# Performance work log

Hardware: AMD Instinct MI355X
Metric: run time of the kernel (lower is better)

Reference implementation:

```python
import jax, jax.numpy as jnp
import numpy as np

V = 50257   # vocab size
E = 256     # embedding_dimension
D = 8       # key_query_reduced_dimensionality
H = 8       # no_of_attention_heads
L = 16      # no_of_blocks
B = 8       # batch
T = 512     # seq len == context_size
FF = 4 * E  # MLP hidden


def setup_inputs() -> dict:
    key = jax.random.key(0)
    ks = jax.random.split(key, 12)
    rn = lambda k, s: jax.random.normal(k, s, jnp.float32) * 0.02
    return {
        'tokens': jax.random.randint(ks[0], (B, T), 0, V),
        'ideal_value': jax.random.randint(ks[1], (B, T), 0, V),
        'tok_emb': rn(ks[2], (V, E)),
        'pos_emb': rn(ks[3], (T, E)),
        'Wq': rn(ks[4], (L, H, E, D)),
        'Wk': rn(ks[5], (L, H, E, D)),
        'Wv': rn(ks[6], (L, H, E, D)),
        'Wo': rn(ks[7], (L, H * D, E)),
        'bo': jnp.zeros((L, E), jnp.float32),
        'ln1_s': jnp.ones((L, E), jnp.float32),
        'ln1_b': jnp.zeros((L, E), jnp.float32),
        'W1': rn(ks[8], (L, E, FF)),
        'b1': jnp.zeros((L, FF), jnp.float32),
        'W2': rn(ks[9], (L, FF, E)),
        'b2': jnp.zeros((L, E), jnp.float32),
        'ln2_s': jnp.ones((L, E), jnp.float32),
        'ln2_b': jnp.zeros((L, E), jnp.float32),
        'lnf_s': jnp.ones((E,), jnp.float32),
        'lnf_b': jnp.zeros((E,), jnp.float32),
        'Wf': rn(ks[10], (E, V)),
        'bf': jnp.zeros((V,), jnp.float32),
    }


def _ln(x, s, b):
    m = x.mean(-1, keepdims=True)
    v = ((x - m) ** 2).mean(-1, keepdims=True)
    return (x - m) * jax.lax.rsqrt(v + 1e-5) * s + b


def reference(tokens, ideal_value, tok_emb, pos_emb, Wq, Wk, Wv, Wo, bo,
              ln1_s, ln1_b, W1, b1, W2, b2, ln2_s, ln2_b, lnf_s, lnf_b, Wf, bf):
    Bn, Tn = tokens.shape
    x = tok_emb[tokens] + pos_emb[:Tn]                      # [B,T,E]
    # faithful mask: masked_fill where transpose(tril(R))==0 -> keep upper triangle
    keep = jnp.triu(jnp.ones((D, D), bool))
    scale = jnp.float32(E) ** 0.5

    def block(x, p):
        wq, wk, wv, wo, bo_, s1, bb1, w1, bm1, w2, bm2, s2, bb2 = p
        h = _ln(x, s1, bb1)
        Q = jnp.einsum('bte,hed->bhtd', h, wq)              # [B,H,T,D]
        K = jnp.einsum('bte,hed->bhtd', h, wk)
        Vv = jnp.einsum('bte,hed->bhtd', h, wv)
        # R = K^T @ Q : feature-by-feature [B,H,D,D] (this repo's quirky attention)
        R = jnp.einsum('bhti,bhtj->bhij', K, Q) / scale
        R = jax.nn.softmax(jnp.where(keep, R, -jnp.inf), axis=-1)
        a = jnp.einsum('bhti,bhij->bhtj', Vv, R)            # V @ R, [B,H,T,D]
        a = a.transpose(0, 2, 1, 3).reshape(x.shape[0], x.shape[1], H * D)
        x = x + a @ wo + bo_                                # dropout is identity (eval)
        h2 = _ln(x, s2, bb2)
        x = x + jax.nn.relu(h2 @ w1 + bm1) @ w2 + bm2
        return x, None

    x, _ = jax.lax.scan(block, x, (Wq, Wk, Wv, Wo, bo, ln1_s, ln1_b,
                                   W1, b1, W2, b2, ln2_s, ln2_b))
    logits = (_ln(x, lnf_s, lnf_b) @ Wf + bf).reshape(-1, V)  # [B*T, V]
    tgt = ideal_value.reshape(-1)
    logp = jax.nn.log_softmax(logits, axis=-1)
    loss = -jnp.take_along_axis(logp, tgt[:, None], axis=1).mean()
    return logits, loss
```

## Files before the change

kernel.cpp:

```cpp
#include <hip/hip_runtime.h>
#include <math.h>

#define V_SZ 50257
#define NPAD 50432
#define NCB 197

typedef short s16x8 __attribute__((ext_vector_type(8)));
typedef ushort u16x4 __attribute__((ext_vector_type(4)));
typedef float f32x4 __attribute__((ext_vector_type(4)));

__device__ __forceinline__ ushort f2bf(float x) {
    union { float f; unsigned u; } v; v.f = x;
    unsigned r = v.u + 0x7FFF + ((v.u >> 16) & 1);
    return (ushort)(r >> 16);
}
__device__ __forceinline__ float bf2f(ushort u) {
    union { unsigned u; float f; } v; v.u = ((unsigned)u) << 16; return v.f;
}

__global__ __launch_bounds__(256) void gpt_embed_ln(const int* __restrict__ tokens,
                                                    const float* __restrict__ tok_emb,
                                                    const float* __restrict__ pos_emb,
                                                    const float* __restrict__ s, const float* __restrict__ b,
                                                    float* __restrict__ x, ushort* __restrict__ hb) {
    int wave = threadIdx.x >> 6, lane = threadIdx.x & 63;
    int row = blockIdx.x * 4 + wave;
    int t = row & 511;
    int tok = tokens[row];
    float4 te = ((const float4*)(tok_emb + tok * 256))[lane];
    float4 pe = ((const float4*)(pos_emb + t * 256))[lane];
    float4 v = make_float4(te.x + pe.x, te.y + pe.y, te.z + pe.z, te.w + pe.w);
    ((float4*)(x + row * 256))[lane] = v;
    float sum = v.x + v.y + v.z + v.w;
    #pragma unroll
    for (int off = 1; off < 64; off <<= 1) sum += __shfl_xor(sum, off);
    float mean = sum * (1.0f / 256.0f);
    float dx = v.x - mean, dy = v.y - mean, dz = v.z - mean, dw = v.w - mean;
    float vs = dx * dx + dy * dy + dz * dz + dw * dw;
    #pragma unroll
    for (int off = 1; off < 64; off <<= 1) vs += __shfl_xor(vs, off);
    float rstd = rsqrtf(vs * (1.0f / 256.0f) + 1e-5f);
    float4 sv = ((const float4*)s)[lane];
    float4 bv = ((const float4*)b)[lane];
    u16x4 o;
    o[0] = f2bf(dx * rstd * sv.x + bv.x);
    o[1] = f2bf(dy * rstd * sv.y + bv.y);
    o[2] = f2bf(dz * rstd * sv.z + bv.z);
    o[3] = f2bf(dw * rstd * sv.w + bv.w);
    *(u16x4*)&hb[row * 256 + lane * 4] = o;
}

__global__ __launch_bounds__(256) void cvt_transpose(const float* __restrict__ in, ushort* __restrict__ out,
                                                     int Kd, int Nd, int n_real,
                                                     int in_stride, int out_stride) {
    __shared__ __align__(16) ushort t[64][80];
    const float* inp = in + (size_t)blockIdx.z * in_stride;
    ushort* outp = out + (size_t)blockIdx.z * out_stride;
    int n0 = blockIdx.x * 64, k0 = blockIdx.y * 64;
    int tid = threadIdx.x;
    #pragma unroll
    for (int p = 0; p < 4; p++) {
        int lk = p * 16 + (tid >> 4);
        int ln = (tid & 15) * 4;
        int k = k0 + lk, n = n0 + ln;
        const float* rowp = inp + (size_t)k * Nd;
        float v0 = 0.f, v1 = 0.f, v2 = 0.f, v3 = 0.f;
        if (n + 0 < n_real) v0 = rowp[n + 0];
        if (n + 1 < n_real) v1 = rowp[n + 1];
        if (n + 2 < n_real) v2 = rowp[n + 2];
        if (n + 3 < n_real) v3 = rowp[n + 3];
        t[ln + 0][lk] = f2bf(v0);
        t[ln + 1][lk] = f2bf(v1);
        t[ln + 2][lk] = f2bf(v2);
        t[ln + 3][lk] = f2bf(v3);
    }
    __syncthreads();
    int ln = tid >> 2, kq = (tid & 3) * 16;
    ushort* op = outp + (size_t)(n0 + ln) * Kd + k0 + kq;
    *(s16x8*)&op[0] = *(const s16x8*)&t[ln][kq];
    *(s16x8*)&op[8] = *(const s16x8*)&t[ln][kq + 8];
}

__global__ __launch_bounds__(256) void cvt_qkv(const float* __restrict__ Wq, const float* __restrict__ Wk,
                                               const float* __restrict__ Wv, ushort* __restrict__ WqkvT) {
    int l = blockIdx.x, kind = blockIdx.y;
    const float* W = (kind == 0 ? Wq : (kind == 1 ? Wk : Wv)) + l * 16384;
    ushort* out = WqkvT + (size_t)l * 65536 + kind * 64 * 256;
    int tid = threadIdx.x;
    #pragma unroll 4
    for (int it = 0; it < 64; it++) {
        int idx = it * 256 + tid;
        int row = idx >> 8, e = idx & 255;
        int h = row >> 3, d = row & 7;
        out[row * 256 + e] = f2bf(W[h * 2048 + e * 8 + d]);
    }
    if (kind == 0) {
        ushort* zp = WqkvT + (size_t)l * 65536 + 192 * 256;
        #pragma unroll 4
        for (int it = 0; it < 64; it++) zp[it * 256 + tid] = 0;
    }
}

__global__ __launch_bounds__(512, 4) void gpt_pre(const ushort* __restrict__ hb,
                                                  const ushort* __restrict__ WqkvT,
                                                  ushort* __restrict__ Vb,
                                                  float* __restrict__ Rpart) {
    __shared__ __align__(16) ushort As[16 * 64];
    __shared__ __align__(16) ushort Bs[256 * 64];
    __shared__ float kqv[16][193];
    const int tid = threadIdx.x, lane = tid & 63, wn = tid >> 6;
    const int rows0 = blockIdx.x * 16;
    const int fr = lane & 15, fkb = (lane >> 4) * 16;
    const int arow = tid >> 3, ach = tid & 7;

    f32x4 acc[2];
    acc[0] = (f32x4)0.0f; acc[1] = (f32x4)0.0f;

    s16x8 ra, rb[4];
    if (tid < 128) ra = *(const s16x8*)&hb[(size_t)(rows0 + arow) * 256 + ach * 8];
    #pragma unroll
    for (int i = 0; i < 4; i++) {
        int u = tid + i * 512, r = u >> 3, ch = u & 7;
        rb[i] = *(const s16x8*)&WqkvT[(size_t)r * 256 + ch * 8];
    }
    #pragma unroll 1
    for (int kt = 0; kt < 4; kt++) {
        if (kt) __syncthreads();
        if (tid < 128)
            *(s16x8*)&As[arow * 64 + (((ach * 16) ^ ((arow & 7) << 4)) >> 1)] = ra;
        #pragma unroll
        for (int i = 0; i < 4; i++) {
            int u = tid + i * 512, r = u >> 3, ch = u & 7;
            *(s16x8*)&Bs[r * 64 + (((ch * 16) ^ ((r & 7) << 4)) >> 1)] = rb[i];
        }
        __syncthreads();
        if (kt < 3) {
            int k0 = (kt + 1) * 64;
            if (tid < 128) ra = *(const s16x8*)&hb[(size_t)(rows0 + arow) * 256 + k0 + ach * 8];
            #pragma unroll
            for (int i = 0; i < 4; i++) {
                int u = tid + i * 512, r = u >> 3, ch = u & 7;
                rb[i] = *(const s16x8*)&WqkvT[(size_t)r * 256 + k0 + ch * 8];
            }
        }
        #pragma unroll
        for (int kk = 0; kk < 2; kk++) {
            int kbyte = kk * 64 + fkb;
            s16x8 af = *(const s16x8*)&As[fr * 64 + ((kbyte ^ ((fr & 7) << 4)) >> 1)];
            #pragma unroll
            for (int n = 0; n < 2; n++) {
                int brow = wn * 32 + n * 16 + fr;
                s16x8 bfv = *(const s16x8*)&Bs[brow * 64 + ((kbyte ^ ((brow & 7) << 4)) >> 1)];
                acc[n] = __builtin_amdgcn_mfma_f32_16x16x32_bf16(af, bfv, acc[n], 0, 0, 0);
            }
        }
    }
    #pragma unroll
    for (int n = 0; n < 2; n++) {
        int col = wn * 32 + n * 16 + fr;
        if (col < 192) {
            #pragma unroll
            for (int r = 0; r < 4; r++)
                kqv[(lane >> 4) * 4 + r][col] = acc[n][r];
        }
    }
    __syncthreads();
    #pragma unroll
    for (int i = 0; i < 2; i++) {
        int u = tid + i * 512, t = u >> 6, hd = u & 63;
        Vb[(size_t)(rows0 + t) * 64 + hd] = f2bf(kqv[t][128 + hd]);
    }
    {
        int h = tid >> 6, i2 = (tid >> 3) & 7, j = tid & 7;
        float s = 0.0f;
        #pragma unroll
        for (int t = 0; t < 16; t++)
            s += kqv[t][64 + h * 8 + i2] * kqv[t][h * 8 + j];
        int bb = rows0 >> 9, part = (rows0 >> 4) & 31;
        Rpart[(size_t)(bb * 32 + part) * 512 + tid] = s;
    }
}

__global__ __launch_bounds__(512, 4) void gpt_layer(
        const float* __restrict__ Rpart_in, const ushort* __restrict__ Vb_in,
        const ushort* __restrict__ WoT, const float* __restrict__ bo,
        const ushort* __restrict__ W1T, const float* __restrict__ b1,
        const ushort* __restrict__ W2T, const float* __restrict__ b2,
        const float* __restrict__ ls2, const float* __restrict__ lb2,
        const float* __restrict__ nls, const float* __restrict__ nlb,
        float* __restrict__ x,
        const ushort* __restrict__ WqkvT_next,
        ushort* __restrict__ Vb_out, float* __restrict__ Rpart_out,
        ushort* __restrict__ hbout, int mode) {
    __shared__ __align__(16) ushort Bs[256 * 64];
    __shared__ __align__(16) ushort ffs[16 * 1024];
    __shared__ __align__(16) ushort h2s[16 * 256];
    __shared__ __align__(16) ushort abl[16 * 64];
    __shared__ __align__(16) ushort Vl[16 * 64];
    __shared__ float Rs[512];
    __shared__ float red1[16][8], red2[16][8], mrow[16], rrow[16];

    const int tid = threadIdx.x, lane = tid & 63, wn = tid >> 6;
    const int rows0 = blockIdx.x * 16, b = rows0 >> 9;
    const int fr = lane & 15, fkb = (lane >> 4) * 16, rbase = (lane >> 4) * 4;
    int colv[2]; colv[0] = wn * 32 + fr; colv[1] = wn * 32 + 16 + fr;

    {
        const float* rp = Rpart_in + (size_t)b * 32 * 512 + tid;
        float s = 0.0f;
        #pragma unroll
        for (int p = 0; p < 32; p++) s += rp[p * 512];
        s *= (1.0f / 16.0f);
        int ii = (tid >> 3) & 7, j = tid & 7;
        float val = (j >= ii) ? s : -INFINITY;
        float m = val;
        #pragma unroll
        for (int off = 1; off < 8; off <<= 1) m = fmaxf(m, __shfl_xor(m, off, 8));
        float ex = __expf(val - m);
        float su = ex;
        #pragma unroll
        for (int off = 1; off < 8; off <<= 1) su += __shfl_xor(su, off, 8);
        Rs[tid] = ex / su;
    }
    #pragma unroll
    for (int i = 0; i < 2; i++) {
        int u = tid + i * 512, t = u >> 6, hd = u & 63;
        Vl[t * 64 + hd] = Vb_in[(size_t)(rows0 + t) * 64 + hd];
    }
    __syncthreads();
    #pragma unroll
    for (int i = 0; i < 2; i++) {
        int u = tid + i * 512, t = u >> 6, hd = u & 63, h = hd >> 3, j = hd & 7;
        float a = 0.0f;
        #pragma unroll
        for (int q = 0; q < 8; q++)
            a += bf2f(Vl[t * 64 + h * 8 + q]) * Rs[h * 64 + q * 8 + j];
        abl[t * 64 + (((hd * 2) ^ ((t & 7) << 4)) >> 1)] = f2bf(a);
    }
    s16x8 rbv[4];
    #pragma unroll
    for (int i = 0; i < 4; i++) {
        int u = tid + i * 512, r = u >> 3, ch = u & 7;
        rbv[i] = *(const s16x8*)&WoT[(size_t)r * 64 + ch * 8];
    }
    __syncthreads();
    #pragma unroll
    for (int i = 0; i < 4; i++) {
        int u = tid + i * 512, r = u >> 3, ch = u & 7;
        *(s16x8*)&Bs[r * 64 + (((ch * 16) ^ ((r & 7) << 4)) >> 1)] = rbv[i];
    }
    __syncthreads();
    f32x4 acc[2];
    acc[0] = (f32x4)0.0f; acc[1] = (f32x4)0.0f;
    #pragma unroll
    for (int kk = 0; kk < 2; kk++) {
        int kbyte = kk * 64 + fkb;
        s16x8 af = *(const s16x8*)&abl[fr * 64 + ((kbyte ^ ((fr & 7) << 4)) >> 1)];
        #pragma unroll
        for (int n = 0; n < 2; n++) {
            int brow = wn * 32 + n * 16 + fr;
            s16x8 bfv = *(const s16x8*)&Bs[brow * 64 + ((kbyte ^ ((brow & 7) << 4)) >> 1)];
            acc[n] = __builtin_amdgcn_mfma_f32_16x16x32_bf16(af, bfv, acc[n], 0, 0, 0);
        }
    }
    float xn[2][4];
    #pragma unroll
    for (int n = 0; n < 2; n++) {
        int col = colv[n];
        float bbv = bo[col];
        #pragma unroll
        for (int r = 0; r < 4; r++)
            xn[n][r] = acc[n][r] + bbv + x[(size_t)(rows0 + rbase + r) * 256 + col];
    }
    #pragma unroll
    for (int r = 0; r < 4; r++) {
        float s1 = xn[0][r] + xn[1][r];
        float s2 = xn[0][r] * xn[0][r] + xn[1][r] * xn[1][r];
        #pragma unroll
        for (int off = 1; off < 16; off <<= 1) {
            s1 += __shfl_xor(s1, off);
            s2 += __shfl_xor(s2, off);
        }
        if (fr == 0) { red1[rbase + r][wn] = s1; red2[rbase + r][wn] = s2; }
    }
    __syncthreads();
    if (tid < 16) {
        float s1 = 0.f, s2 = 0.f;
        #pragma unroll
        for (int w = 0; w < 8; w++) { s1 += red1[tid][w]; s2 += red2[tid][w]; }
        float mean = s1 * (1.0f / 256.0f);
        float var = s2 * (1.0f / 256.0f) - mean * mean;
        mrow[tid] = mean;
        rrow[tid] = rsqrtf(var + 1e-5f);
    }
    __syncthreads();
    #pragma unroll
    for (int n = 0; n < 2; n++) {
        int col = colv[n];
        float lsv = ls2[col], lbv = lb2[col];
        #pragma unroll
        for (int r = 0; r < 4; r++) {
            int rl = rbase + r;
            float hv = (xn[n][r] - mrow[rl]) * rrow[rl] * lsv + lbv;
            h2s[rl * 256 + (((col * 2) ^ ((rl & 7) << 4)) >> 1)] = f2bf(hv);
        }
    }
    #pragma unroll 1
    for (int c = 0; c < 4; c++) {
        const ushort* Bg = W1T + (size_t)c * 256 * 256;
        acc[0] = (f32x4)0.0f; acc[1] = (f32x4)0.0f;
        #pragma unroll
        for (int i = 0; i < 4; i++) {
            int u = tid + i * 512, r = u >> 3, ch = u & 7;
            rbv[i] = *(const s16x8*)&Bg[(size_t)r * 256 + ch * 8];
        }
        #pragma unroll 1
        for (int kt = 0; kt < 4; kt++) {
            __syncthreads();
            #pragma unroll
            for (int i = 0; i < 4; i++) {
                int u = tid + i * 512, r = u >> 3, ch = u & 7;
                *(s16x8*)&Bs[r * 64 + (((ch * 16) ^ ((r & 7) << 4)) >> 1)] = rbv[i];
            }
            __syncthreads();
            if (kt < 3) {
                int k0 = (kt + 1) * 64;
                #pragma unroll
                for (int i = 0; i < 4; i++) {
                    int u = tid + i * 512, r = u >> 3, ch = u & 7;
                    rbv[i] = *(const s16x8*)&Bg[(size_t)r * 256 + k0 + ch * 8];
                }
            }
            #pragma unroll
            for (int kk = 0; kk < 2; kk++) {
                int kbyte = kt * 128 + kk * 64 + fkb;
                s16x8 af = *(const s16x8*)&h2s[fr * 256 + ((kbyte ^ ((fr & 7) << 4)) >> 1)];
                int kb2 = kk * 64 + fkb;
                #pragma unroll
                for (int n = 0; n < 2; n++) {
                    int brow = wn * 32 + n * 16 + fr;
                    s16x8 bfv = *(const s16x8*)&Bs[brow * 64 + ((kb2 ^ ((brow & 7) << 4)) >> 1)];
                    acc[n] = __builtin_amdgcn_mfma_f32_16x16x32_bf16(af, bfv, acc[n], 0, 0, 0);
                }
            }
        }
        #pragma unroll
        for (int n = 0; n < 2; n++) {
            int col = c * 256 + colv[n];
            float bb1 = b1[col];
            #pragma unroll
            for (int r = 0; r < 4; r++) {
                int rl = rbase + r;
                ffs[rl * 1024 + (((col * 2) ^ ((rl & 7) << 4)) >> 1)] =
                    f2bf(fmaxf(acc[n][r] + bb1, 0.0f));
            }
        }
    }
    f32x4 a2[2];
    a2[0] = (f32x4)0.0f; a2[1] = (f32x4)0.0f;
    #pragma unroll
    for (int i = 0; i < 4; i++) {
        int u = tid + i * 512, r = u >> 3, ch = u & 7;
        rbv[i] = *(const s16x8*)&W2T[(size_t)r * 1024 + ch * 8];
    }
    #pragma unroll 1
    for (int kt = 0; kt < 16; kt++) {
        __syncthreads();
        #pragma unroll
        for (int i = 0; i < 4; i++) {
            int u = tid + i * 512, r = u >> 3, ch = u & 7;
            *(s16x8*)&Bs[r * 64 + (((ch * 16) ^ ((r & 7) << 4)) >> 1)] = rbv[i];
        }
        __syncthreads();
        if (kt < 15) {
            int k0 = (kt + 1) * 64;
            #pragma unroll
            for (int i = 0; i < 4; i++) {
                int u = tid + i * 512, r = u >> 3, ch = u & 7;
                rbv[i] = *(const s16x8*)&W2T[(size_t)r * 1024 + k0 + ch * 8];
            }
        }
        #pragma unroll
        for (int kk = 0; kk < 2; kk++) {
            int kbyte = kt * 128 + kk * 64 + fkb;
            s16x8 af = *(const s16x8*)&ffs[fr * 1024 + ((kbyte ^ ((fr & 7) << 4)) >> 1)];
            int kb2 = kk * 64 + fkb;
            #pragma unroll
            for (int n = 0; n < 2; n++) {
                int brow = wn * 32 + n * 16 + fr;
                s16x8 bfv = *(const s16x8*)&Bs[brow * 64 + ((kb2 ^ ((brow & 7) << 4)) >> 1)];
                a2[n] = __builtin_amdgcn_mfma_f32_16x16x32_bf16(af, bfv, a2[n], 0, 0, 0);
            }
        }
    }
    #pragma unroll
    for (int n = 0; n < 2; n++) {
        int col = colv[n];
        float bb2 = b2[col];
        #pragma unroll
        for (int r = 0; r < 4; r++) {
            float v = xn[n][r] + a2[n][r] + bb2;
            xn[n][r] = v;
            x[(size_t)(rows0 + rbase + r) * 256 + col] = v;
        }
    }
    __syncthreads();
    #pragma unroll
    for (int r = 0; r < 4; r++) {
        float s1 = xn[0][r] + xn[1][r];
        float s2 = xn[0][r] * xn[0][r] + xn[1][r] * xn[1][r];
        #pragma unroll
        for (int off = 1; off < 16; off <<= 1) {
            s1 += __shfl_xor(s1, off);
            s2 += __shfl_xor(s2, off);
        }
        if (fr == 0) { red1[rbase + r][wn] = s1; red2[rbase + r][wn] = s2; }
    }
    __syncthreads();
    if (tid < 16) {
        float s1 = 0.f, s2 = 0.f;
        #pragma unroll
        for (int w = 0; w < 8; w++) { s1 += red1[tid][w]; s2 += red2[tid][w]; }
        float mean = s1 * (1.0f / 256.0f);
        float var = s2 * (1.0f / 256.0f) - mean * mean;
        mrow[tid] = mean;
        rrow[tid] = rsqrtf(var + 1e-5f);
    }
    __syncthreads();
    #pragma unroll
    for (int n = 0; n < 2; n++) {
        int col = colv[n];
        float lsv = nls[col], lbv = nlb[col];
        #pragma unroll
        for (int r = 0; r < 4; r++) {
            int rl = rbase + r;
            float hv = (xn[n][r] - mrow[rl]) * rrow[rl] * lsv + lbv;
            ushort hu = f2bf(hv);
            h2s[rl * 256 + (((col * 2) ^ ((rl & 7) << 4)) >> 1)] = hu;
            if (mode == 0)
                hbout[(size_t)(rows0 + rl) * 256 + col] = hu;
        }
    }
    if (mode == 0) return;

    float* kqv = (float*)ffs;
    acc[0] = (f32x4)0.0f; acc[1] = (f32x4)0.0f;
    #pragma unroll
    for (int i = 0; i < 4; i++) {
        int u = tid + i * 512, r = u >> 3, ch = u & 7;
        rbv[i] = *(const s16x8*)&WqkvT_next[(size_t)r * 256 + ch * 8];
    }
    #pragma unroll 1
    for (int kt = 0; kt < 4; kt++) {
        __syncthreads();
        #pragma unroll
        for (int i = 0; i < 4; i++) {
            int u = tid + i * 512, r = u >> 3, ch = u & 7;
            *(s16x8*)&Bs[r * 64 + (((ch * 16) ^ ((r & 7) << 4)) >> 1)] = rbv[i];
        }
        __syncthreads();
        if (kt < 3) {
            int k0 = (kt + 1) * 64;
            #pragma unroll
            for (int i = 0; i < 4; i++) {
                int u = tid + i * 512, r = u >> 3, ch = u & 7;
                rbv[i] = *(const s16x8*)&WqkvT_next[(size_t)r * 256 + k0 + ch * 8];
            }
        }
        #pragma unroll
        for (int kk = 0; kk < 2; kk++) {
            int kbyte = kt * 128 + kk * 64 + fkb;
            s16x8 af = *(const s16x8*)&h2s[fr * 256 + ((kbyte ^ ((fr & 7) << 4)) >> 1)];
            int kb2 = kk * 64 + fkb;
            #pragma unroll
            for (int n = 0; n < 2; n++) {
                int brow = wn * 32 + n * 16 + fr;
                s16x8 bfv = *(const s16x8*)&Bs[brow * 64 + ((kb2 ^ ((brow & 7) << 4)) >> 1)];
                acc[n] = __builtin_amdgcn_mfma_f32_16x16x32_bf16(af, bfv, acc[n], 0, 0, 0);
            }
        }
    }
    __syncthreads();
    #pragma unroll
    for (int n = 0; n < 2; n++) {
        int col = wn * 32 + n * 16 + fr;
        if (col < 192) {
            #pragma unroll
            for (int r = 0; r < 4; r++)
                kqv[(rbase + r) * 193 + col] = acc[n][r];
        }
    }
    __syncthreads();
    #pragma unroll
    for (int i = 0; i < 2; i++) {
        int u = tid + i * 512, t = u >> 6, hd = u & 63;
        Vb_out[(size_t)(rows0 + t) * 64 + hd] = f2bf(kqv[t * 193 + 128 + hd]);
    }
    {
        int h = tid >> 6, i2 = (tid >> 3) & 7, j = tid & 7;
        float s = 0.0f;
        #pragma unroll
        for (int t = 0; t < 16; t++)
            s += kqv[t * 193 + 64 + h * 8 + i2] * kqv[t * 193 + h * 8 + j];
        int part = (rows0 >> 4) & 31;
        Rpart_out[(size_t)(b * 32 + part) * 512 + tid] = s;
    }
}

__global__ __launch_bounds__(512, 4) void gpt_logits_mfma(const ushort* __restrict__ hb, const ushort* __restrict__ WfT,
                                                          const float* __restrict__ bfb, float* __restrict__ out,
                                                          float2* __restrict__ lsebuf) {
    __shared__ __align__(16) ushort As[128 * 64];
    __shared__ __align__(16) ushort Bs[256 * 64];
    f32x4 acc[4][4];
    int flat = blockIdx.y * 32 + blockIdx.x;
    int nf = (flat & 7) * 788 + (flat >> 3);
    int rb = nf & 31, cb = nf >> 5;
    int row0 = rb * 128, c0 = cb * 256;
    const int tid = threadIdx.x, lane = tid & 63, wid = tid >> 6;
    const int wm = wid >> 2, wn = wid & 3;
    const int fr = lane & 15, fkb = (lane >> 4) * 16;

    #pragma unroll
    for (int m = 0; m < 4; m++)
        #pragma unroll
        for (int n = 0; n < 4; n++) acc[m][n] = (f32x4)0.0f;

    s16x8 ra[2], rbv[4];
    #pragma unroll
    for (int i = 0; i < 2; i++) {
        int u = tid + i * 512, r = u >> 3, ch = u & 7;
        ra[i] = *(const s16x8*)&hb[(size_t)(row0 + r) * 256 + ch * 8];
    }
    #pragma unroll
    for (int i = 0; i < 4; i++) {
        int u = tid + i * 512, r = u >> 3, ch = u & 7;
        rbv[i] = *(const s16x8*)&WfT[(size_t)(c0 + r) * 256 + ch * 8];
    }
    #pragma unroll 1
    for (int kt = 0; kt < 4; kt++) {
        if (kt) __syncthreads();
        #pragma unroll
        for (int i = 0; i < 2; i++) {
            int u = tid + i * 512, r = u >> 3, ch = u & 7;
            *(s16x8*)&As[r * 64 + (((ch * 16) ^ ((r & 7) << 4)) >> 1)] = ra[i];
        }
        #pragma unroll
        for (int i = 0; i < 4; i++) {
            int u = tid + i * 512, r = u >> 3, ch = u & 7;
            *(s16x8*)&Bs[r * 64 + (((ch * 16) ^ ((r & 7) << 4)) >> 1)] = rbv[i];
        }
        __syncthreads();
        if (kt < 3) {
            int k0 = (kt + 1) * 64;
            #pragma unroll
            for (int i = 0; i < 2; i++) {
                int u = tid + i * 512, r = u >> 3, ch = u & 7;
                ra[i] = *(const s16x8*)&hb[(size_t)(row0 + r) * 256 + k0 + ch * 8];
            }
            #pragma unroll
            for (int i = 0; i < 4; i++) {
                int u = tid + i * 512, r = u >> 3, ch = u & 7;
                rbv[i] = *(const s16x8*)&WfT[(size_t)(c0 + r) * 256 + k0 + ch * 8];
            }
        }
        #pragma unroll
        for (int kk = 0; kk < 2; kk++) {
            int kbyte = kk * 64 + fkb;
            s16x8 af[4], bfr[4];
            #pragma unroll
            for (int m = 0; m < 4; m++) {
                int arow = wm * 64 + m * 16 + fr;
                af[m] = *(const s16x8*)&As[arow * 64 + ((kbyte ^ ((arow & 7) << 4)) >> 1)];
            }
            #pragma unroll
            for (int n = 0; n < 4; n++) {
                int brow = wn * 64 + n * 16 + fr;
                bfr[n] = *(const s16x8*)&Bs[brow * 64 + ((kbyte ^ ((brow & 7) << 4)) >> 1)];
            }
            #pragma unroll
            for (int m = 0; m < 4; m++)
                #pragma unroll
                for (int n = 0; n < 4; n++)
                    acc[m][n] = __builtin_amdgcn_mfma_f32_16x16x32_bf16(af[m], bfr[n], acc[m][n], 0, 0, 0);
        }
    }
    float bb[4]; int gcv[4];
    #pragma unroll
    for (int n = 0; n < 4; n++) {
        int gc = c0 + wn * 64 + n * 16 + fr;
        gcv[n] = gc;
        bb[n] = (gc < V_SZ) ? bfb[gc] : 0.0f;
    }
    __syncthreads();
    float2 (*red)[4] = (float2(*)[4])As;
    #pragma unroll
    for (int m = 0; m < 4; m++) {
        int rloc = wm * 64 + m * 16 + (lane >> 4) * 4;
        int gr = row0 + rloc;
        #pragma unroll
        for (int r = 0; r < 4; r++) {
            float v[4];
            float vmax = -1e30f;
            #pragma unroll
            for (int n = 0; n < 4; n++) {
                v[n] = (gcv[n] < V_SZ) ? acc[m][n][r] + bb[n] : -1e30f;
                vmax = fmaxf(vmax, v[n]);
            }
            #pragma unroll
            for (int n = 0; n < 4; n++)
                if (gcv[n] < V_SZ)
                    out[(size_t)(gr + r) * V_SZ + gcv[n]] = v[n];
            #pragma unroll
            for (int off = 1; off < 16; off <<= 1)
                vmax = fmaxf(vmax, __shfl_xor(vmax, off));
            float vsum = __expf(v[0] - vmax) + __expf(v[1] - vmax)
                       + __expf(v[2] - vmax) + __expf(v[3] - vmax);
            #pragma unroll
            for (int off = 1; off < 16; off <<= 1)
                vsum += __shfl_xor(vsum, off);
            if ((lane & 15) == 0)
                red[rloc + r][wn] = make_float2(vmax, vsum);
        }
    }
    __syncthreads();
    if (tid < 128) {
        float M = -1e30f, S = 0.0f;
        #pragma unroll
        for (int w = 0; w < 4; w++) {
            float2 p = red[tid][w];
            float M2 = fmaxf(M, p.x);
            S = S * __expf(M - M2) + p.y * __expf(p.x - M2);
            M = M2;
        }
        lsebuf[(size_t)(row0 + tid) * NCB + cb] = make_float2(M, S);
    }
}

__global__ __launch_bounds__(256) void gpt_lse(const float2* __restrict__ lsebuf, const float* __restrict__ out,
                                               const int* __restrict__ tgt, float* __restrict__ partial) {
    int wave = threadIdx.x >> 6, lane = threadIdx.x & 63;
    int row = blockIdx.x * 4 + wave;
    float m = -INFINITY, s = 0.0f;
    for (int i = lane; i < NCB; i += 64) {
        float2 p = lsebuf[(size_t)row * NCB + i];
        float M = fmaxf(m, p.x);
        s = s * __expf(m - M) + p.y * __expf(p.x - M);
        m = M;
    }
    #pragma unroll
    for (int off = 1; off < 64; off <<= 1) {
        float m2 = __shfl_xor(m, off);
        float s2 = __shfl_xor(s, off);
        float M = fmaxf(m, m2);
        s = s * __expf(m - M) + s2 * __expf(m2 - M);
        m = M;
    }
    if (lane == 0)
        partial[row] = m + logf(s) - out[(size_t)row * V_SZ + tgt[row]];
}

__global__ void gpt_loss_reduce(const float* __restrict__ partial, float* __restrict__ out) {
    __shared__ float red[256];
    int tid = threadIdx.x;
    float s = 0.0f;
    for (int i = tid; i < 4096; i += 256) s += partial[i];
    red[tid] = s;
    __syncthreads();
    for (int off = 128; off > 0; off >>= 1) {
        if (tid < off) red[tid] += red[tid + off];
        __syncthreads();
    }
    if (tid == 0) out[0] = red[0] * (1.0f / 4096.0f);
}

__global__ void gpt_embed(const int* __restrict__ tokens, const float* __restrict__ tok_emb,
                          const float* __restrict__ pos_emb, float* __restrict__ x) {
    int idx = blockIdx.x * 256 + threadIdx.x;
    int bt = idx >> 8, e = idx & 255;
    int t = bt & 511;
    int tok = tokens[bt];
    x[idx] = tok_emb[tok * 256 + e] + pos_emb[t * 256 + e];
}

__global__ void gpt_ln(const float* __restrict__ x, const float* __restrict__ s,
                       const float* __restrict__ b, float* __restrict__ h) {
    __shared__ float red[256];
    int row = blockIdx.x, e = threadIdx.x;
    float v = x[row * 256 + e];
    red[e] = v;
    __syncthreads();
    for (int off = 128; off > 0; off >>= 1) {
        if (e < off) red[e] += red[e + off];
        __syncthreads();
    }
    float mean = red[0] * (1.0f / 256.0f);
    __syncthreads();
    float d = v - mean;
    red[e] = d * d;
    __syncthreads();
    for (int off = 128; off > 0; off >>= 1) {
        if (e < off) red[e] += red[e + off];
        __syncthreads();
    }
    float rstd = rsqrtf(red[0] * (1.0f / 256.0f) + 1e-5f);
    h[row * 256 + e] = d * rstd * s[e] + b[e];
}

__global__ void gpt_qkv(const float* __restrict__ h, const float* __restrict__ Wq,
                        const float* __restrict__ Wk, const float* __restrict__ Wv,
                        float* __restrict__ Q, float* __restrict__ K, float* __restrict__ Vv) {
    __shared__ float hs[8][256];
    int tid = threadIdx.x;
    int row0 = blockIdx.x * 8;
    #pragma unroll
    for (int r = 0; r < 8; r++) hs[r][tid] = h[(row0 + r) * 256 + tid];
    __syncthreads();
    if (tid < 192) {
        int kind = tid >> 6, o = tid & 63, hh = o >> 3, d = o & 7;
        const float* W = kind == 0 ? Wq : (kind == 1 ? Wk : Wv);
        const float* wp = W + hh * 2048 + d;
        float acc[8];
        #pragma unroll
        for (int r = 0; r < 8; r++) acc[r] = 0.0f;
        for (int e = 0; e < 256; e++) {
            float w = wp[e * 8];
            #pragma unroll
            for (int r = 0; r < 8; r++) acc[r] += hs[r][e] * w;
        }
        float* outp = kind == 0 ? Q : (kind == 1 ? K : Vv);
        int b = row0 >> 9;
        #pragma unroll
        for (int r = 0; r < 8; r++) {
            int t = (row0 + r) & 511;
            outp[((b * 8 + hh) * 512 + t) * 8 + d] = acc[r];
        }
    }
}

__global__ void gpt_attn_r(const float* __restrict__ K, const float* __restrict__ Q,
                           float* __restrict__ R) {
    __shared__ __align__(16) float Ks[64][8];
    __shared__ __align__(16) float Qs[64][8];
    int bh = blockIdx.x, tid = threadIdx.x;
    int i = tid >> 3, j = tid & 7;
    const float* Kb = K + bh * 512 * 8;
    const float* Qb = Q + bh * 512 * 8;
    float acc = 0.0f;
    for (int t0 = 0; t0 < 512; t0 += 64) {
        *(float4*)&Ks[tid][0] = *(const float4*)&Kb[(t0 + tid) * 8];
        *(float4*)&Ks[tid][4] = *(const float4*)&Kb[(t0 + tid) * 8 + 4];
        *(float4*)&Qs[tid][0] = *(const float4*)&Qb[(t0 + tid) * 8];
        *(float4*)&Qs[tid][4] = *(const float4*)&Qb[(t0 + tid) * 8 + 4];
        __syncthreads();
        #pragma unroll 16
        for (int t = 0; t < 64; t++) acc += Ks[t][i] * Qs[t][j];
        __syncthreads();
    }
    acc *= (1.0f / 16.0f);
    float val = (j >= i) ? acc : -INFINITY;
    float m = val;
    #pragma unroll
    for (int off = 1; off < 8; off <<= 1) m = fmaxf(m, __shfl_xor(m, off, 8));
    float ex = expf(val - m);
    float sum = ex;
    #pragma unroll
    for (int off = 1; off < 8; off <<= 1) sum += __shfl_xor(sum, off, 8);
    R[bh * 64 + tid] = ex / sum;
}

__global__ void gpt_attn_out(const float* __restrict__ Vv, const float* __restrict__ R,
                             const float* __restrict__ Wo, const float* __restrict__ bo,
                             float* __restrict__ x) {
    __shared__ __align__(16) float as[8][64];
    int tid = threadIdx.x;
    int row0 = blockIdx.x * 8;
    int b = row0 >> 9;
    #pragma unroll
    for (int k = 0; k < 2; k++) {
        int idx = k * 256 + tid;
        int r = idx >> 6, hd = idx & 63;
        int hh = hd >> 3, jj = hd & 7;
        int t = (row0 + r) & 511;
        const float* vp = Vv + ((b * 8 + hh) * 512 + t) * 8;
        const float* rp = R + (b * 8 + hh) * 64 + jj;
        float a = 0.0f;
        #pragma unroll
        for (int i = 0; i < 8; i++) a += vp[i] * rp[i * 8];
        as[r][hd] = a;
    }
    __syncthreads();
    float acc[8];
    float bb = bo[tid];
    #pragma unroll
    for (int r = 0; r < 8; r++) acc[r] = bb;
    for (int hd0 = 0; hd0 < 64; hd0 += 4) {
        float w0 = Wo[(hd0 + 0) * 256 + tid];
        float w1 = Wo[(hd0 + 1) * 256 + tid];
        float w2 = Wo[(hd0 + 2) * 256 + tid];
        float w3 = Wo[(hd0 + 3) * 256 + tid];
        #pragma unroll
        for (int r = 0; r < 8; r++) {
            float4 av = *(const float4*)&as[r][hd0];
            acc[r] += av.x * w0 + av.y * w1 + av.z * w2 + av.w * w3;
        }
    }
    #pragma unroll
    for (int r = 0; r < 8; r++) x[(row0 + r) * 256 + tid] += acc[r];
}

__global__ __launch_bounds__(256) void gpt_mlp(const float* __restrict__ h, const float* __restrict__ W1,
                         const float* __restrict__ b1, const float* __restrict__ W2,
                         const float* __restrict__ b2, float* __restrict__ x) {
    __shared__ __align__(16) float hs[8][256];
    __shared__ __align__(16) float ffs[8][1024];
    int tid = threadIdx.x;
    int row0 = blockIdx.x * 8;
    #pragma unroll
    for (int r = 0; r < 8; r++) hs[r][tid] = h[(row0 + r) * 256 + tid];
    __syncthreads();
    {
        float acc[4][8];
        #pragma unroll
        for (int k = 0; k < 4; k++) {
            float bb = b1[k * 256 + tid];
            #pragma unroll
            for (int r = 0; r < 8; r++) acc[k][r] = bb;
        }
        for (int e0 = 0; e0 < 256; e0 += 4) {
            float w[4][4];
            #pragma unroll
            for (int ee = 0; ee < 4; ee++)
                #pragma unroll
                for (int k = 0; k < 4; k++)
                    w[ee][k] = W1[(e0 + ee) * 1024 + k * 256 + tid];
            #pragma unroll
            for (int r = 0; r < 8; r++) {
                float4 hv = *(const float4*)&hs[r][e0];
                #pragma unroll
                for (int k = 0; k < 4; k++)
                    acc[k][r] += hv.x * w[0][k] + hv.y * w[1][k] + hv.z * w[2][k] + hv.w * w[3][k];
            }
        }
        #pragma unroll
        for (int k = 0; k < 4; k++)
            #pragma unroll
            for (int r = 0; r < 8; r++)
                ffs[r][k * 256 + tid] = fmaxf(acc[k][r], 0.0f);
    }
    __syncthreads();
    {
        float acc[8];
        float bb = b2[tid];
        #pragma unroll
        for (int r = 0; r < 8; r++) acc[r] = bb;
        for (int f0 = 0; f0 < 1024; f0 += 4) {
            float w0 = W2[(f0 + 0) * 256 + tid];
            float w1 = W2[(f0 + 1) * 256 + tid];
            float w2 = W2[(f0 + 2) * 256 + tid];
            float w3 = W2[(f0 + 3) * 256 + tid];
            #pragma unroll
            for (int r = 0; r < 8; r++) {
                float4 fv = *(const float4*)&ffs[r][f0];
                acc[r] += fv.x * w0 + fv.y * w1 + fv.z * w2 + fv.w * w3;
            }
        }
        #pragma unroll
        for (int r = 0; r < 8; r++) x[(row0 + r) * 256 + tid] += acc[r];
    }
}

__global__ __launch_bounds__(256) void gpt_logits(const float* __restrict__ hf, const float* __restrict__ Wf,
                            const float* __restrict__ bf, float* __restrict__ out) {
    __shared__ __align__(16) float hs[32][256];
    int tid = threadIdx.x;
    int row0 = blockIdx.y * 32;
    #pragma unroll
    for (int r = 0; r < 32; r++) hs[r][tid] = hf[(row0 + r) * 256 + tid];
    __syncthreads();
    int c0 = blockIdx.x * 512 + tid;
    int c1 = c0 + 256;
    int c0c = c0 < V_SZ ? c0 : V_SZ - 1;
    int c1c = c1 < V_SZ ? c1 : V_SZ - 1;
    float acc0[32], acc1[32];
    float b0 = bf[c0c], b1 = bf[c1c];
    #pragma unroll
    for (int r = 0; r < 32; r++) { acc0[r] = b0; acc1[r] = b1; }
    const float* p0 = Wf + c0c;
    const float* p1 = Wf + c1c;
    for (int e0 = 0; e0 < 256; e0 += 4) {
        float w00 = p0[(size_t)(e0 + 0) * V_SZ];
        float w01 = p0[(size_t)(e0 + 1) * V_SZ];
        float w02 = p0[(size_t)(e0 + 2) * V_SZ];
        float w03 = p0[(size_t)(e0 + 3) * V_SZ];
        float w10 = p1[(size_t)(e0 + 0) * V_SZ];
        float w11 = p1[(size_t)(e0 + 1) * V_SZ];
        float w12 = p1[(size_t)(e0 + 2) * V_SZ];
        float w13 = p1[(size_t)(e0 + 3) * V_SZ];
        #pragma unroll
        for (int r = 0; r < 32; r++) {
            float4 hv = *(const float4*)&hs[r][e0];
            acc0[r] += hv.x * w00 + hv.y * w01 + hv.z * w02 + hv.w * w03;
            acc1[r] += hv.x * w10 + hv.y * w11 + hv.z * w12 + hv.w * w13;
        }
    }
    if (c0 < V_SZ) {
        #pragma unroll
        for (int r = 0; r < 32; r++) out[(size_t)(row0 + r) * V_SZ + c0] = acc0[r];
    }
    if (c1 < V_SZ) {
        #pragma unroll
        for (int r = 0; r < 32; r++) out[(size_t)(row0 + r) * V_SZ + c1] = acc1[r];
    }
}

__global__ void gpt_loss(const float* __restrict__ logits, const int* __restrict__ tgt,
                         float* __restrict__ partial) {
    __shared__ float ms[256], ss[256];
    int row = blockIdx.x, tid = threadIdx.x;
    const float* lr = logits + (size_t)row * V_SZ;
    float m = -INFINITY, s = 0.0f;
    for (int c = tid; c < V_SZ; c += 256) {
        float v = lr[c];
        float nm = fmaxf(m, v);
        s = s * expf(m - nm) + expf(v - nm);
        m = nm;
    }
    ms[tid] = m; ss[tid] = s;
    __syncthreads();
    for (int off = 128; off > 0; off >>= 1) {
        if (tid < off) {
            float m2 = ms[tid + off], s2 = ss[tid + off];
            float M = fmaxf(ms[tid], m2);
            ss[tid] = ss[tid] * expf(ms[tid] - M) + s2 * expf(m2 - M);
            ms[tid] = M;
        }
        __syncthreads();
    }
    if (tid == 0) {
        float lse = ms[0] + logf(ss[0]);
        partial[row] = lse - lr[tgt[row]];
    }
}

extern "C" void kernel_launch(void* const* d_in, const int* in_sizes, int n_in,
                              void* d_out, int out_size, void* d_ws, size_t ws_size,
                              hipStream_t stream) {
    const int*   tokens  = (const int*)d_in[0];
    const int*   ideal   = (const int*)d_in[1];
    const float* tok_emb = (const float*)d_in[2];
    const float* pos_emb = (const float*)d_in[3];
    const float* Wq      = (const float*)d_in[4];
    const float* Wk      = (const float*)d_in[5];
    const float* Wv      = (const float*)d_in[6];
    const float* Wo      = (const float*)d_in[7];
    const float* bo      = (const float*)d_in[8];
    const float* ln1_s   = (const float*)d_in[9];
    const float* ln1_b   = (const float*)d_in[10];
    const float* W1      = (const float*)d_in[11];
    const float* b1      = (const float*)d_in[12];
    const float* W2      = (const float*)d_in[13];
    const float* b2      = (const float*)d_in[14];
    const float* ln2_s   = (const float*)d_in[15];
    const float* ln2_b   = (const float*)d_in[16];
    const float* lnf_s   = (const float*)d_in[17];
    const float* lnf_b   = (const float*)d_in[18];
    const float* Wf      = (const float*)d_in[19];
    const float* bf      = (const float*)d_in[20];
    float* out = (float*)d_out;

    size_t off = 0;
    char* wsc = (char*)d_ws;
    ushort* WfT   = (ushort*)(wsc + off); off += (size_t)NPAD * 256 * 2;
    ushort* W1T   = (ushort*)(wsc + off); off += (size_t)16 * 1024 * 256 * 2;
    ushort* W2T   = (ushort*)(wsc + off); off += (size_t)16 * 256 * 1024 * 2;
    ushort* WqkvT = (ushort*)(wsc + off); off += (size_t)16 * 256 * 256 * 2;
    ushort* WoT   = (ushort*)(wsc + off); off += (size_t)16 * 256 * 64 * 2;
    ushort* hb    = (ushort*)(wsc + off); off += (size_t)4096 * 256 * 2;
    ushort* Vb0   = (ushort*)(wsc + off); off += (size_t)4096 * 64 * 2;
    ushort* Vb1   = (ushort*)(wsc + off); off += (size_t)4096 * 64 * 2;
    float*  x     = (float*)(wsc + off);  off += (size_t)4096 * 256 * 4;
    float*  Rp0   = (float*)(wsc + off);  off += (size_t)8 * 32 * 512 * 4;
    float*  Rp1   = (float*)(wsc + off);  off += (size_t)8 * 32 * 512 * 4;
    float*  partial = (float*)(wsc + off); off += (size_t)4096 * 4;
    float2* lsebuf = (float2*)(wsc + off); off += (size_t)4096 * NCB * 8;
    bool big = ws_size >= off;

    if (big) {
        cvt_transpose<<<dim3(16, 4, 16), 256, 0, stream>>>(W1, W1T, 256, 1024, 1024, 262144, 262144);
        cvt_transpose<<<dim3(4, 16, 16), 256, 0, stream>>>(W2, W2T, 1024, 256, 256, 262144, 262144);
        cvt_transpose<<<dim3(4, 1, 16), 256, 0, stream>>>(Wo, WoT, 64, 256, 256, 16384, 16384);
        cvt_transpose<<<dim3(788, 4, 1), 256, 0, stream>>>(Wf, WfT, 256, V_SZ, V_SZ, 0, 0);
        cvt_qkv<<<dim3(16, 3), 256, 0, stream>>>(Wq, Wk, Wv, WqkvT);

        gpt_embed_ln<<<1024, 256, 0, stream>>>(tokens, tok_emb, pos_emb, ln1_s, ln1_b, x, hb);
        gpt_pre<<<256, 512, 0, stream>>>(hb, WqkvT, Vb0, Rp0);

        for (int l = 0; l < 16; l++) {
            const float* nls = (l < 15) ? ln1_s + (l + 1) * 256 : lnf_s;
            const float* nlb = (l < 15) ? ln1_b + (l + 1) * 256 : lnf_b;
            const float* Rin = (l & 1) ? Rp1 : Rp0;
            const ushort* Vin = (l & 1) ? Vb1 : Vb0;
            float* Rout = (l & 1) ? Rp0 : Rp1;
            ushort* Vout = (l & 1) ? Vb0 : Vb1;
            int mode = (l < 15) ? 1 : 0;
            const ushort* Wnext = WqkvT + (size_t)((l < 15) ? (l + 1) : 0) * 65536;
            gpt_layer<<<256, 512, 0, stream>>>(Rin, Vin,
                                               WoT + (size_t)l * 16384, bo + l * 256,
                                               W1T + (size_t)l * 262144, b1 + l * 1024,
                                               W2T + (size_t)l * 262144, b2 + l * 256,
                                               ln2_s + l * 256, ln2_b + l * 256,
                                               nls, nlb, x,
                                               Wnext, Vout, Rout, hb, mode);
        }

        gpt_logits_mfma<<<dim3(32, NCB), 512, 0, stream>>>(hb, WfT, bf, out, lsebuf);
        gpt_lse<<<1024, 256, 0, stream>>>(lsebuf, out, ideal, partial);
        gpt_loss_reduce<<<1, 256, 0, stream>>>(partial, out + (size_t)4096 * V_SZ);
    } else {
        float* fx  = (float*)d_ws;
        float* fh  = fx + 4096 * 256;
        float* fQ  = fh + 4096 * 256;
        float* fK  = fQ + 4096 * 64;
        float* fV  = fK + 4096 * 64;
        float* fR  = fV + 4096 * 64;
        float* fpart = fR + 64 * 64;
        gpt_embed<<<4096, 256, 0, stream>>>(tokens, tok_emb, pos_emb, fx);
        for (int l = 0; l < 16; l++) {
            gpt_ln<<<4096, 256, 0, stream>>>(fx, ln1_s + l * 256, ln1_b + l * 256, fh);
            gpt_qkv<<<512, 256, 0, stream>>>(fh, Wq + l * 16384, Wk + l * 16384, Wv + l * 16384, fQ, fK, fV);
            gpt_attn_r<<<64, 64, 0, stream>>>(fK, fQ, fR);
            gpt_attn_out<<<512, 256, 0, stream>>>(fV, fR, Wo + l * 16384, bo + l * 256, fx);
            gpt_ln<<<4096, 256, 0, stream>>>(fx, ln2_s + l * 256, ln2_b + l * 256, fh);
            gpt_mlp<<<512, 256, 0, stream>>>(fh, W1 + l * 262144, b1 + l * 1024, W2 + l * 262144, b2 + l * 256, fx);
        }
        gpt_ln<<<4096, 256, 0, stream>>>(fx, lnf_s, lnf_b, fh);
        dim3 lg(99, 128);
        gpt_logits<<<lg, 256, 0, stream>>>(fh, Wf, bf, out);
        gpt_loss<<<4096, 256, 0, stream>>>(out, ideal, fpart);
        gpt_loss_reduce<<<1, 256, 0, stream>>>(fpart, out + (size_t)4096 * V_SZ);
    }
}
```

Baseline: 1.002 ms.

## Load weight MFMA fragments directly from global memory instead of LDS staging

Removes the shared-memory B tile (Bs) and its register-prefetch/store/barrier pipeline in the fused layer kernel. Each wave now reads its own B fragments straight from global/L2 for the Wo, W1, W2 and next-layer QKV GEMMs. This drops many __syncthreads and 32KB of LDS, which could raise occupancy. The cost is that each weight fragment is fetched from cache per wave with uncoalesced 16-byte loads and no latency hiding beyond what the compiler schedules.

Measured after the change: 1.171 ms. +16.9%, slower.

```diff
diff --git a/kernel.cpp b/kernel.cpp
--- a/kernel.cpp
+++ b/kernel.cpp
@@ -192,7 +192,6 @@
         const ushort* __restrict__ WqkvT_next,
         ushort* __restrict__ Vb_out, float* __restrict__ Rpart_out,
         ushort* __restrict__ hbout, int mode) {
-    __shared__ __align__(16) ushort Bs[256 * 64];
     __shared__ __align__(16) ushort ffs[16 * 1024];
     __shared__ __align__(16) ushort h2s[16 * 256];
     __shared__ __align__(16) ushort abl[16 * 64];
@@ -203,7 +202,9 @@
     const int tid = threadIdx.x, lane = tid & 63, wn = tid >> 6;
     const int rows0 = blockIdx.x * 16, b = rows0 >> 9;
     const int fr = lane & 15, fkb = (lane >> 4) * 16, rbase = (lane >> 4) * 4;
+    const int koffe = (lane >> 4) * 8;
     int colv[2]; colv[0] = wn * 32 + fr; colv[1] = wn * 32 + 16 + fr;
+    const int brow0 = wn * 32 + fr, brow1 = wn * 32 + 16 + fr;
 
     {
         const float* rp = Rpart_in + (size_t)b * 32 * 512 + tid;
@@ -237,18 +238,6 @@
             a += bf2f(Vl[t * 64 + h * 8 + q]) * Rs[h * 64 + q * 8 + j];
         abl[t * 64 + (((hd * 2) ^ ((t & 7) << 4)) >> 1)] = f2bf(a);
     }
-    s16x8 rbv[4];
-    #pragma unroll
-    for (int i = 0; i < 4; i++) {
-        int u = tid + i * 512, r = u >> 3, ch = u & 7;
-        rbv[i] = *(const s16x8*)&WoT[(size_t)r * 64 + ch * 8];
-    }
-    __syncthreads();
-    #pragma unroll
-    for (int i = 0; i < 4; i++) {
-        int u = tid + i * 512, r = u >> 3, ch = u & 7;
-        *(s16x8*)&Bs[r * 64 + (((ch * 16) ^ ((r & 7) << 4)) >> 1)] = rbv[i];
-    }
     __syncthreads();
     f32x4 acc[2];
     acc[0] = (f32x4)0.0f; acc[1] = (f32x4)0.0f;
@@ -256,12 +245,10 @@
     for (int kk = 0; kk < 2; kk++) {
         int kbyte = kk * 64 + fkb;
         s16x8 af = *(const s16x8*)&abl[fr * 64 + ((kbyte ^ ((fr & 7) << 4)) >> 1)];
-        #pragma unroll
-        for (int n = 0; n < 2; n++) {
-            int brow = wn * 32 + n * 16 + fr;
-            s16x8 bfv = *(const s16x8*)&Bs[brow * 64 + ((kbyte ^ ((brow & 7) << 4)) >> 1)];
-            acc[n] = __builtin_amdgcn_mfma_f32_16x16x32_bf16(af, bfv, acc[n], 0, 0, 0);
-        }
+        s16x8 b0 = *(const s16x8*)&WoT[(size_t)brow0 * 64 + kk * 32 + koffe];
+        s16x8 b1v = *(const s16x8*)&WoT[(size_t)brow1 * 64 + kk * 32 + koffe];
+        acc[0] = __builtin_amdgcn_mfma_f32_16x16x32_bf16(af, b0, acc[0], 0, 0, 0);
+        acc[1] = __builtin_amdgcn_mfma_f32_16x16x32_bf16(af, b1v, acc[1], 0, 0, 0);
     }
     float xn[2][4];
     #pragma unroll
@@ -305,43 +292,22 @@
             h2s[rl * 256 + (((col * 2) ^ ((rl & 7) << 4)) >> 1)] = f2bf(hv);
         }
     }
+    __syncthreads();
     #pragma unroll 1
     for (int c = 0; c < 4; c++) {
         const ushort* Bg = W1T + (size_t)c * 256 * 256;
         acc[0] = (f32x4)0.0f; acc[1] = (f32x4)0.0f;
         #pragma unroll
-        for (int i = 0; i < 4; i++) {
-            int u = tid + i * 512, r = u >> 3, ch = u & 7;
-            rbv[i] = *(const s16x8*)&Bg[(size_t)r * 256 + ch * 8];
-        }
-        #pragma unroll 1
         for (int kt = 0; kt < 4; kt++) {
-            __syncthreads();
-            #pragma unroll
-            for (int i = 0; i < 4; i++) {
-                int u = tid + i * 512, r = u >> 3, ch = u & 7;
-                *(s16x8*)&Bs[r * 64 + (((ch * 16) ^ ((r & 7) << 4)) >> 1)] = rbv[i];
-            }
-            __syncthreads();
-            if (kt < 3) {
-                int k0 = (kt + 1) * 64;
-                #pragma unroll
-                for (int i = 0; i < 4; i++) {
-                    int u = tid + i * 512, r = u >> 3, ch = u & 7;
-                    rbv[i] = *(const s16x8*)&Bg[(size_t)r * 256 + k0 + ch * 8];
-                }
-            }
             #pragma unroll
             for (int kk = 0; kk < 2; kk++) {
                 int kbyte = kt * 128 + kk * 64 + fkb;
                 s16x8 af = *(const s16x8*)&h2s[fr * 256 + ((kbyte ^ ((fr & 7) << 4)) >> 1)];
-                int kb2 = kk * 64 + fkb;
-                #pragma unroll
-                for (int n = 0; n < 2; n++) {
-                    int brow = wn * 32 + n * 16 + fr;
-                    s16x8 bfv = *(const s16x8*)&Bs[brow * 64 + ((kb2 ^ ((brow & 7) << 4)) >> 1)];
-                    acc[n] = __builtin_amdgcn_mfma_f32_16x16x32_bf16(af, bfv, acc[n], 0, 0, 0);
-                }
+                int ke = kt * 64 + kk * 32 + koffe;
+                s16x8 b0 = *(const s16x8*)&Bg[(size_t)brow0 * 256 + ke];
+                s16x8 b1v = *(const s16x8*)&Bg[(size_t)brow1 * 256 + ke];
+                acc[0] = __builtin_amdgcn_mfma_f32_16x16x32_bf16(af, b0, acc[0], 0, 0, 0);
+                acc[1] = __builtin_amdgcn_mfma_f32_16x16x32_bf16(af, b1v, acc[1], 0, 0, 0);
             }
         }
         #pragma unroll
@@ -356,41 +322,20 @@
             }
         }
     }
+    __syncthreads();
     f32x4 a2[2];
     a2[0] = (f32x4)0.0f; a2[1] = (f32x4)0.0f;
-    #pragma unroll
-    for (int i = 0; i < 4; i++) {
-        int u = tid + i * 512, r = u >> 3, ch = u & 7;
-        rbv[i] = *(const s16x8*)&W2T[(size_t)r * 1024 + ch * 8];
-    }
-    #pragma unroll 1
+    #pragma unroll 4
     for (int kt = 0; kt < 16; kt++) {
-        __syncthreads();
-        #pragma unroll
-        for (int i = 0; i < 4; i++) {
-            int u = tid + i * 512, r = u >> 3, ch = u & 7;
-            *(s16x8*)&Bs[r * 64 + (((ch * 16) ^ ((r & 7) << 4)) >> 1)] = rbv[i];
-        }
-        __syncthreads();
-        if (kt < 15) {
-            int k0 = (kt + 1) * 64;
-            #pragma unroll
-            for (int i = 0; i < 4; i++) {
-                int u = tid + i * 512, r = u >> 3, ch = u & 7;
-                rbv[i] = *(const s16x8*)&W2T[(size_t)r * 1024 + k0 + ch * 8];
-            }
-        }
         #pragma unroll
         for (int kk = 0; kk < 2; kk++) {
             int kbyte = kt * 128 + kk * 64 + fkb;
             s16x8 af = *(const s16x8*)&ffs[fr * 1024 + ((kbyte ^ ((fr & 7) << 4)) >> 1)];
-            int kb2 = kk * 64 + fkb;
-            #pragma unroll
-            for (int n = 0; n < 2; n++) {
-                int brow = wn * 32 + n * 16 + fr;
-                s16x8 bfv = *(const s16x8*)&Bs[brow * 64 + ((kb2 ^ ((brow & 7) << 4)) >> 1)];
-                a2[n] = __builtin_amdgcn_mfma_f32_16x16x32_bf16(af, bfv, a2[n], 0, 0, 0);
-            }
+            int ke = kt * 64 + kk * 32 + koffe;
+            s16x8 b0 = *(const s16x8*)&W2T[(size_t)brow0 * 1024 + ke];
+            s16x8 b1v = *(const s16x8*)&W2T[(size_t)brow1 * 1024 + ke];
+            a2[0] = __builtin_amdgcn_mfma_f32_16x16x32_bf16(af, b0, a2[0], 0, 0, 0);
+            a2[1] = __builtin_amdgcn_mfma_f32_16x16x32_bf16(af, b1v, a2[1], 0, 0, 0);
         }
     }
     #pragma unroll
@@ -442,42 +387,21 @@
         }
     }
     if (mode == 0) return;
+    __syncthreads();
 
     float* kqv = (float*)ffs;
     acc[0] = (f32x4)0.0f; acc[1] = (f32x4)0.0f;
     #pragma unroll
-    for (int i = 0; i < 4; i++) {
-        int u = tid + i * 512, r = u >> 3, ch = u & 7;
-        rbv[i] = *(const s16x8*)&WqkvT_next[(size_t)r * 256 + ch * 8];
-    }
-    #pragma unroll 1
     for (int kt = 0; kt < 4; kt++) {
-        __syncthreads();
-        #pragma unroll
-        for (int i = 0; i < 4; i++) {
-            int u = tid + i * 512, r = u >> 3, ch = u & 7;
-            *(s16x8*)&Bs[r * 64 + (((ch * 16) ^ ((r & 7) << 4)) >> 1)] = rbv[i];
-        }
-        __syncthreads();
-        if (kt < 3) {
-            int k0 = (kt + 1) * 64;
-            #pragma unroll
-            for (int i = 0; i < 4; i++) {
-                int u = tid + i * 512, r = u >> 3, ch = u & 7;
-                rbv[i] = *(const s16x8*)&WqkvT_next[(size_t)r * 256 + k0 + ch * 8];
-            }
-        }
         #pragma unroll
         for (int kk = 0; kk < 2; kk++) {
             int kbyte = kt * 128 + kk * 64 + fkb;
             s16x8 af = *(const s16x8*)&h2s[fr * 256 + ((kbyte ^ ((fr & 7) << 4)) >> 1)];
-            int kb2 = kk * 64 + fkb;
-            #pragma unroll
-            for (int n = 0; n < 2; n++) {
-                int brow = wn * 32 + n * 16 + fr;
-                s16x8 bfv = *(const s16x8*)&Bs[brow * 64 + ((kb2 ^ ((brow & 7) << 4)) >> 1)];
-                acc[n] = __builtin_amdgcn_mfma_f32_16x16x32_bf16(af, bfv, acc[n], 0, 0, 0);
-            }
+            int ke = kt * 64 + kk * 32 + koffe;
+            s16x8 b0 = *(const s16x8*)&WqkvT_next[(size_t)brow0 * 256 + ke];
+            s16x8 b1v = *(const s16x8*)&WqkvT_next[(size_t)brow1 * 256 + ke];
+            acc[0] = __builtin_amdgcn_mfma_f32_16x16x32_bf16(af, b0, acc[0], 0, 0, 0);
+            acc[1] = __builtin_amdgcn_mfma_f32_16x16x32_bf16(af, b1v, acc[1], 0, 0, 0);
         }
     }
     __syncthreads();
```
